# Performance work log

Measured on AMD Instinct MI355X. Metric: run time of the kernel, lower is better.

## Reference

```python
import jax, jax.numpy as jnp
import numpy as np

B, L, D = 4, 4096, 256
INIT_ALPHA = -2.0
INV_TEMP = 1.0 / 0.1


def setup_inputs() -> dict:
    key = jax.random.key(0)
    k1, k2, k3, k4 = jax.random.split(key, 4)
    latents = jax.random.normal(k1, (B, L, D), dtype=jnp.float32)
    current_coords = jax.random.normal(k2, (B, L, 2), dtype=jnp.float32)
    # Linear(D, D, bias=False) weights (torch stores [out, in]; y = x @ W.T)
    lim = 1.0 / np.sqrt(D)
    Wq = jax.random.uniform(k3, (D, D), minval=-lim, maxval=lim, dtype=jnp.float32)
    Wk = jax.random.uniform(k4, (D, D), minval=-lim, maxval=lim, dtype=jnp.float32)
    alpha_raw = jnp.asarray(INIT_ALPHA, dtype=jnp.float32)
    return {"latents": latents, "current_coords": current_coords,
            "Wq": Wq, "Wk": Wk, "alpha_raw": alpha_raw, "layer_idx": 3}


def _l2norm(x, eps=1e-12):
    # F.normalize(dim=-1): x / max(||x||, eps)
    n = jnp.sqrt(jnp.sum(x * x, axis=-1, keepdims=True))
    return x / jnp.maximum(n, eps)


def reference(latents, current_coords, Wq, Wk, alpha_raw, layer_idx):
    # pred_idx selection (share_weights=True): 0 if layer_idx==0 else 1;
    # layer_idx=3 -> params given are for pred_idx=1.
    q = _l2norm(jnp.einsum('bld,ed->ble', latents, Wq))  # [B,L,D]
    k = _l2norm(jnp.einsum('bld,ed->ble', latents, Wk))  # [B,L,D]
    scores = jnp.einsum('bld,bmd->blm', q, k) * INV_TEMP  # [B,L,L]
    scores = jnp.clip(scores, -50.0, 50.0)
    W = jax.nn.softmax(scores, axis=-1)                   # [B,L,L]
    alpha = jax.nn.sigmoid(alpha_raw)
    # M = alpha*W + (1-alpha)*I; M @ coords == alpha*(W@coords) + (1-alpha)*coords
    new_coords = alpha * jnp.einsum('blm,bmc->blc', W, current_coords) \
                 + (1.0 - alpha) * current_coords
    displacement = new_coords - current_coords
    return (new_coords, displacement)
```

## Files before the change

### kernel.cpp

```cpp
#include <hip/hip_runtime.h>
#include <hip/hip_bf16.h>

#define BB 4
#define LL 4096
#define DD 256
#define MM (BB * LL)
#define NSPLIT 4
#define NQB (LL / 128)
#define KPS (LL / NSPLIT)
#define KT 64
#define NKT (KPS / KT)

typedef short short8 __attribute__((ext_vector_type(8)));
typedef float floatx4 __attribute__((ext_vector_type(4)));

#define SCALE_LOG2E 14.426950408889634f

__device__ __forceinline__ unsigned short f2bf(float f) {
    __hip_bfloat16 h = __float2bfloat16(f);
    union { __hip_bfloat16 h; unsigned short s; } c; c.h = h; return c.s;
}

__device__ __forceinline__ float fast_exp2(float x) {
#if __has_builtin(__builtin_amdgcn_exp2f)
    return __builtin_amdgcn_exp2f(x);
#else
    return exp2f(x);
#endif
}

__device__ __forceinline__ void stage16(const char* g, char* l, int lane) {
#if __has_builtin(__builtin_amdgcn_global_load_lds)
    __builtin_amdgcn_global_load_lds(
        (const __attribute__((address_space(1))) void*)(g + lane * 16),
        (__attribute__((address_space(3))) void*)l, 16, 0, 0);
#else
    *(short8*)(l + lane * 16) = *(const short8*)(g + lane * 16);
#endif
}

__global__ __launch_bounds__(256) void cvt_swz_kernel(
    const float* __restrict__ srcq, const float* __restrict__ srck,
    unsigned short* __restrict__ dstq, unsigned short* __restrict__ dstk)
{
    const int which = blockIdx.x >> 5;
    const float* src = which ? srck : srcq;
    unsigned short* dst = which ? dstk : dstq;
    const int t = (blockIdx.x & 31) * 256 + threadIdx.x;
    const int r = t >> 5, c = t & 31;
    const float4 v0 = ((const float4*)src)[t * 2];
    const float4 v1 = ((const float4*)src)[t * 2 + 1];
    short8 o;
    o[0] = (short)f2bf(v0.x); o[1] = (short)f2bf(v0.y);
    o[2] = (short)f2bf(v0.z); o[3] = (short)f2bf(v0.w);
    o[4] = (short)f2bf(v1.x); o[5] = (short)f2bf(v1.y);
    o[6] = (short)f2bf(v1.z); o[7] = (short)f2bf(v1.w);
    const int cs = c ^ (r & 7);
    *(short8*)(dst + (size_t)r * DD + cs * 8) = o;
}

__global__ __launch_bounds__(256) void proj_norm_kernel(
    const float* __restrict__ latents,
    const __hip_bfloat16* __restrict__ Wq,
    const __hip_bfloat16* __restrict__ Wk,
    __hip_bfloat16* __restrict__ qn,
    __hip_bfloat16* __restrict__ kn)
{
    __shared__ char lds[65536];

    const int tid  = threadIdx.x;
    const int wave = tid >> 6;
    const int lane = tid & 63;
    const int n15  = lane & 15;
    const int quad = lane >> 4;
    const int sw   = n15 & 7;

    const int pass  = blockIdx.x & 1;
    const int rbase = (blockIdx.x >> 1) * 64;
    const int m0    = rbase + wave * 16;
    const int r160  = rbase >> 4;

    short8 afrag[8];
    const float* Abase = latents + (size_t)(m0 + n15) * DD + quad * 8;
#pragma unroll
    for (int kk = 0; kk < 8; ++kk) {
        const float4 v0 = *(const float4*)(Abase + kk * 32);
        const float4 v1 = *(const float4*)(Abase + kk * 32 + 4);
        short8 f;
        f[0] = (short)f2bf(v0.x); f[1] = (short)f2bf(v0.y);
        f[2] = (short)f2bf(v0.z); f[3] = (short)f2bf(v0.w);
        f[4] = (short)f2bf(v1.x); f[5] = (short)f2bf(v1.y);
        f[6] = (short)f2bf(v1.z); f[7] = (short)f2bf(v1.w);
        afrag[kk] = f;
    }

    const char* W = (const char*)(pass ? Wk : Wq);

    floatx4 acc[16];
#pragma unroll
    for (int ct = 0; ct < 16; ++ct) acc[ct] = (floatx4){0.f, 0.f, 0.f, 0.f};

    {
        const char* src = W + wave * 8192;
        char* dst = lds + wave * 8192;
#pragma unroll
        for (int j = 0; j < 8; ++j) stage16(src + j * 1024, dst + j * 1024, lane);
    }

    for (int round = 0; round < 4; ++round) {
        __syncthreads();
        if (round + 1 < 4) {
            const char* src = W + (size_t)(round + 1) * 32768 + wave * 8192;
            char* dst = lds + ((round + 1) & 1) * 32768 + wave * 8192;
#pragma unroll
            for (int j = 0; j < 8; ++j) stage16(src + j * 1024, dst + j * 1024, lane);
        }
        const char* buf = lds + (round & 1) * 32768;
#pragma unroll
        for (int jt = 0; jt < 4; ++jt) {
            const int ct = round * 4 + jt;
            const char* lbase = buf + (jt * 16 + n15) * 512;
            floatx4 a = acc[ct];
#pragma unroll
            for (int kk = 0; kk < 8; ++kk) {
                const int chunk = (4 * kk + quad) ^ sw;
                short8 bfr = *(const short8*)(lbase + chunk * 16);
                a = __builtin_amdgcn_mfma_f32_16x16x32_bf16(afrag[kk], bfr, a, 0, 0, 0);
            }
            acc[ct] = a;
        }
    }

    float ss[4] = {0.f, 0.f, 0.f, 0.f};
#pragma unroll
    for (int ct = 0; ct < 16; ++ct)
#pragma unroll
        for (int r = 0; r < 4; ++r) ss[r] += acc[ct][r] * acc[ct][r];
#pragma unroll
    for (int r = 0; r < 4; ++r) {
        ss[r] += __shfl_xor(ss[r], 1, 64);
        ss[r] += __shfl_xor(ss[r], 2, 64);
        ss[r] += __shfl_xor(ss[r], 4, 64);
        ss[r] += __shfl_xor(ss[r], 8, 64);
    }
    float sc[4];
#pragma unroll
    for (int r = 0; r < 4; ++r) {
        sc[r] = 1.f / fmaxf(sqrtf(ss[r]), 1e-12f);
        if (pass == 0) sc[r] *= SCALE_LOG2E;
    }

    unsigned short* tb = (unsigned short*)lds;
#pragma unroll
    for (int h = 0; h < 2; ++h) {
        __syncthreads();
#pragma unroll
        for (int cth = 0; cth < 8; ++cth) {
            const int ct = h * 8 + cth;
            const int col = cth * 16 + n15;
#pragma unroll
            for (int r = 0; r < 4; ++r) {
                const int rl = wave * 16 + quad * 4 + r;
                tb[rl * 136 + col] = f2bf(acc[ct][r] * sc[r]);
            }
        }
        __syncthreads();
        if (pass == 0) {
#pragma unroll
            for (int j = 0; j < 4; ++j) {
                const int g = tid + j * 256;
                const int n15r = g & 15, q2 = (g >> 4) & 3, kkh = (g >> 6) & 3, r16l = (g >> 8) & 3;
                const int rl = r16l * 16 + n15r;
                short8 v = *(const short8*)(tb + rl * 136 + kkh * 32 + q2 * 8);
                const size_t chunk = (((size_t)(r160 + r16l) * 8 + (h * 4 + kkh)) * 4 + q2) * 16 + n15r;
                *(short8*)((char*)qn + chunk * 16) = v;
            }
        } else {
#pragma unroll
            for (int j = 0; j < 4; ++j) {
                const int g = tid + j * 256;
                const int csl = g & 15, rl = g >> 4;
                const int row = rbase + rl;
                const int ci = csl ^ (row & 7);
                short8 v = *(const short8*)(tb + rl * 136 + ci * 8);
                *(short8*)((char*)kn + (size_t)row * 512 + (h * 16 + csl) * 16) = v;
            }
        }
    }
}

__global__ __launch_bounds__(256) void attn_kernel(
    const __hip_bfloat16* __restrict__ qn,
    const __hip_bfloat16* __restrict__ kn,
    const float* __restrict__ coords,
    float* __restrict__ partials)
{
    __shared__ char lds[2 * 32768];

    const int tid  = threadIdx.x;
    const int wave = tid >> 6;
    const int lane = tid & 63;
    const int n15  = lane & 15;
    const int quad = lane >> 4;
    const int sw   = n15 & 7;

    int bs = blockIdx.x;
    const int qb    = bs % NQB;    bs /= NQB;
    const int split = bs % NSPLIT; bs /= NSPLIT;
    const int b     = bs;

    const int mw = b * LL + qb * 128 + wave * 32;

    const int key_base = b * LL + split * KPS;
    const char* ksrc = (const char*)kn + (size_t)key_base * 512;

    {
        const char* src = ksrc + wave * 8192;
        char* dst = lds + wave * 8192;
#pragma unroll
        for (int j = 0; j < 8; ++j) stage16(src + j * 1024, dst + j * 1024, lane);
    }

    short8 aq[2][8];
    const int t16 = mw >> 4;
#pragma unroll
    for (int rt = 0; rt < 2; ++rt)
#pragma unroll
        for (int kk = 0; kk < 8; ++kk) {
            const size_t chunk = (((size_t)(t16 + rt) * 8 + kk) * 4 + quad) * 16 + n15;
            aq[rt][kk] = *(const short8*)((const char*)qn + chunk * 16);
        }

    float s0[2][4], s1[2][4], s2[2][4];
#pragma unroll
    for (int rt = 0; rt < 2; ++rt)
#pragma unroll
        for (int r = 0; r < 4; ++r) { s0[rt][r] = 0.f; s1[rt][r] = 0.f; s2[rt][r] = 0.f; }

    for (int kt = 0; kt < NKT; ++kt) {
        __syncthreads();
        if (kt + 1 < NKT) {
            const char* src = ksrc + (size_t)(kt + 1) * KT * 512 + wave * 8192;
            char* dst = lds + ((kt + 1) & 1) * 32768 + wave * 8192;
#pragma unroll
            for (int j = 0; j < 8; ++j) stage16(src + j * 1024, dst + j * 1024, lane);
        }
        const char* buf = lds + (kt & 1) * 32768;

#pragma unroll
        for (int ct = 0; ct < 4; ++ct) {
            const int kidx = key_base + kt * KT + ct * 16 + n15;
            const float2 cc = *(const float2*)(coords + (size_t)kidx * 2);

            floatx4 acc0 = (floatx4){0.f, 0.f, 0.f, 0.f};
            floatx4 acc1 = (floatx4){0.f, 0.f, 0.f, 0.f};
            const char* lbase = buf + (ct * 16 + n15) * 512;
#pragma unroll
            for (int kk = 0; kk < 8; ++kk) {
                const int chunk = (4 * kk + quad) ^ sw;
                short8 bfr = *(const short8*)(lbase + chunk * 16);
                acc0 = __builtin_amdgcn_mfma_f32_16x16x32_bf16(aq[0][kk], bfr, acc0, 0, 0, 0);
                acc1 = __builtin_amdgcn_mfma_f32_16x16x32_bf16(aq[1][kk], bfr, acc1, 0, 0, 0);
            }
#pragma unroll
            for (int r = 0; r < 4; ++r) {
                const float e0 = fast_exp2(acc0[r]);
                const float e1 = fast_exp2(acc1[r]);
                s0[0][r] += e0;
                s1[0][r] = fmaf(cc.x, e0, s1[0][r]);
                s2[0][r] = fmaf(cc.y, e0, s2[0][r]);
                s0[1][r] += e1;
                s1[1][r] = fmaf(cc.x, e1, s1[1][r]);
                s2[1][r] = fmaf(cc.y, e1, s2[1][r]);
            }
        }
    }

#pragma unroll
    for (int rt = 0; rt < 2; ++rt)
#pragma unroll
        for (int r = 0; r < 4; ++r)
#pragma unroll
            for (int mask = 1; mask <= 8; mask <<= 1) {
                s0[rt][r] += __shfl_xor(s0[rt][r], mask, 64);
                s1[rt][r] += __shfl_xor(s1[rt][r], mask, 64);
                s2[rt][r] += __shfl_xor(s2[rt][r], mask, 64);
            }

    if (n15 == 0) {
#pragma unroll
        for (int rt = 0; rt < 2; ++rt)
#pragma unroll
            for (int r = 0; r < 4; ++r) {
                const int m = mw + rt * 16 + quad * 4 + r;
                float* p = partials + ((size_t)split * MM + m) * 4;
                p[0] = s0[rt][r];
                p[1] = s1[rt][r];
                p[2] = s2[rt][r];
            }
    }
}

__global__ __launch_bounds__(256) void finish_kernel(
    const float* __restrict__ partials,
    const float* __restrict__ coords,
    const float* __restrict__ alpha_raw,
    float* __restrict__ out)
{
    const int m = blockIdx.x * 256 + threadIdx.x;

    const float alpha = 1.f / (1.f + __expf(-alpha_raw[0]));

    float s0 = 0.f, s1 = 0.f, s2 = 0.f;
#pragma unroll
    for (int s = 0; s < NSPLIT; ++s) {
        const float4 v = *(const float4*)(partials + ((size_t)s * MM + m) * 4);
        s0 += v.x; s1 += v.y; s2 += v.z;
    }

    const float cx = coords[m * 2];
    const float cy = coords[m * 2 + 1];
    const float inv = 1.f / s0;
    const float nx = alpha * (s1 * inv) + (1.f - alpha) * cx;
    const float ny = alpha * (s2 * inv) + (1.f - alpha) * cy;

    out[m * 2]     = nx;
    out[m * 2 + 1] = ny;
    out[2 * MM + m * 2]     = nx - cx;
    out[2 * MM + m * 2 + 1] = ny - cy;
}

extern "C" void kernel_launch(void* const* d_in, const int* in_sizes, int n_in,
                              void* d_out, int out_size, void* d_ws, size_t ws_size,
                              hipStream_t stream) {
    const float* latents   = (const float*)d_in[0];
    const float* coords    = (const float*)d_in[1];
    const float* Wq        = (const float*)d_in[2];
    const float* Wk        = (const float*)d_in[3];
    const float* alpha_raw = (const float*)d_in[4];

    char* ws = (char*)d_ws;
    __hip_bfloat16* qn   = (__hip_bfloat16*)ws;
    __hip_bfloat16* kn   = (__hip_bfloat16*)(ws + (size_t)8 * 1024 * 1024);
    __hip_bfloat16* wq_b = (__hip_bfloat16*)(ws + (size_t)16 * 1024 * 1024);
    __hip_bfloat16* wk_b = (__hip_bfloat16*)(ws + (size_t)16 * 1024 * 1024 + 131072);
    float* partials      = (float*)(ws + (size_t)16 * 1024 * 1024 + 262144);

    float* out = (float*)d_out;

    cvt_swz_kernel<<<64, 256, 0, stream>>>(Wq, Wk, (unsigned short*)wq_b, (unsigned short*)wk_b);
    proj_norm_kernel<<<512, 256, 0, stream>>>(latents, wq_b, wk_b, qn, kn);
    attn_kernel<<<BB * NQB * NSPLIT, 256, 0, stream>>>(qn, kn, coords, partials);
    finish_kernel<<<MM / 256, 256, 0, stream>>>(partials, coords, alpha_raw, out);
}
```

Baseline: 124.9 us.

## Read projection weights directly from global and double attention key splits

The projection kernel stops staging swizzled weights through a 64KB LDS double buffer. Each wave now reads bf16 weight rows straight from global memory (L2-resident), and the weight conversion kernel drops the swizzle. The attention kernel doubles the key splits to 8 and halves the key tile to 32, which doubles the grid and halves LDS per block to raise occupancy. The risk is more partials for the finish kernel to reduce and uncoalesced global loads of B fragments in the projection.

```diff
diff --git a/kernel.cpp b/kernel.cpp
--- a/kernel.cpp
+++ b/kernel.cpp
@@ -5,10 +5,10 @@
 #define LL 4096
 #define DD 256
 #define MM (BB * LL)
-#define NSPLIT 4
+#define NSPLIT 8
 #define NQB (LL / 128)
 #define KPS (LL / NSPLIT)
-#define KT 64
+#define KT 32
 #define NKT (KPS / KT)
 
 typedef short short8 __attribute__((ext_vector_type(8)));
@@ -39,7 +39,7 @@
 #endif
 }
 
-__global__ __launch_bounds__(256) void cvt_swz_kernel(
+__global__ __launch_bounds__(256) void cvt_kernel(
     const float* __restrict__ srcq, const float* __restrict__ srck,
     unsigned short* __restrict__ dstq, unsigned short* __restrict__ dstk)
 {
@@ -47,7 +47,6 @@
     const float* src = which ? srck : srcq;
     unsigned short* dst = which ? dstk : dstq;
     const int t = (blockIdx.x & 31) * 256 + threadIdx.x;
-    const int r = t >> 5, c = t & 31;
     const float4 v0 = ((const float4*)src)[t * 2];
     const float4 v1 = ((const float4*)src)[t * 2 + 1];
     short8 o;
@@ -55,8 +54,7 @@
     o[2] = (short)f2bf(v0.z); o[3] = (short)f2bf(v0.w);
     o[4] = (short)f2bf(v1.x); o[5] = (short)f2bf(v1.y);
     o[6] = (short)f2bf(v1.z); o[7] = (short)f2bf(v1.w);
-    const int cs = c ^ (r & 7);
-    *(short8*)(dst + (size_t)r * DD + cs * 8) = o;
+    *(short8*)(dst + (size_t)t * 8) = o;
 }
 
 __global__ __launch_bounds__(256) void proj_norm_kernel(
@@ -66,14 +64,13 @@
     __hip_bfloat16* __restrict__ qn,
     __hip_bfloat16* __restrict__ kn)
 {
-    __shared__ char lds[65536];
+    __shared__ unsigned short tb[64 * 136];
 
     const int tid  = threadIdx.x;
     const int wave = tid >> 6;
     const int lane = tid & 63;
     const int n15  = lane & 15;
     const int quad = lane >> 4;
-    const int sw   = n15 & 7;
 
     const int pass  = blockIdx.x & 1;
     const int rbase = (blockIdx.x >> 1) * 64;
@@ -94,41 +91,22 @@
         afrag[kk] = f;
     }
 
-    const char* W = (const char*)(pass ? Wk : Wq);
+    const short* W = (const short*)(pass ? Wk : Wq);
 
     floatx4 acc[16];
 #pragma unroll
     for (int ct = 0; ct < 16; ++ct) acc[ct] = (floatx4){0.f, 0.f, 0.f, 0.f};
 
-    {
-        const char* src = W + wave * 8192;
-        char* dst = lds + wave * 8192;
-#pragma unroll
-        for (int j = 0; j < 8; ++j) stage16(src + j * 1024, dst + j * 1024, lane);
-    }
-
-    for (int round = 0; round < 4; ++round) {
-        __syncthreads();
-        if (round + 1 < 4) {
-            const char* src = W + (size_t)(round + 1) * 32768 + wave * 8192;
-            char* dst = lds + ((round + 1) & 1) * 32768 + wave * 8192;
-#pragma unroll
-            for (int j = 0; j < 8; ++j) stage16(src + j * 1024, dst + j * 1024, lane);
-        }
-        const char* buf = lds + (round & 1) * 32768;
-#pragma unroll
-        for (int jt = 0; jt < 4; ++jt) {
-            const int ct = round * 4 + jt;
-            const char* lbase = buf + (jt * 16 + n15) * 512;
-            floatx4 a = acc[ct];
-#pragma unroll
-            for (int kk = 0; kk < 8; ++kk) {
-                const int chunk = (4 * kk + quad) ^ sw;
-                short8 bfr = *(const short8*)(lbase + chunk * 16);
-                a = __builtin_amdgcn_mfma_f32_16x16x32_bf16(afrag[kk], bfr, a, 0, 0, 0);
-            }
-            acc[ct] = a;
-        }
+#pragma unroll
+    for (int ct = 0; ct < 16; ++ct) {
+        const short* Brow = W + (size_t)(ct * 16 + n15) * DD + quad * 8;
+        floatx4 a = acc[ct];
+#pragma unroll
+        for (int kk = 0; kk < 8; ++kk) {
+            short8 bfr = *(const short8*)(Brow + kk * 32);
+            a = __builtin_amdgcn_mfma_f32_16x16x32_bf16(afrag[kk], bfr, a, 0, 0, 0);
+        }
+        acc[ct] = a;
     }
 
     float ss[4] = {0.f, 0.f, 0.f, 0.f};
@@ -150,7 +128,6 @@
         if (pass == 0) sc[r] *= SCALE_LOG2E;
     }
 
-    unsigned short* tb = (unsigned short*)lds;
 #pragma unroll
     for (int h = 0; h < 2; ++h) {
         __syncthreads();
@@ -195,7 +172,7 @@
     const float* __restrict__ coords,
     float* __restrict__ partials)
 {
-    __shared__ char lds[2 * 32768];
+    __shared__ char lds[2 * 16384];
 
     const int tid  = threadIdx.x;
     const int wave = tid >> 6;
@@ -215,10 +192,10 @@
     const char* ksrc = (const char*)kn + (size_t)key_base * 512;
 
     {
-        const char* src = ksrc + wave * 8192;
-        char* dst = lds + wave * 8192;
-#pragma unroll
-        for (int j = 0; j < 8; ++j) stage16(src + j * 1024, dst + j * 1024, lane);
+        const char* src = ksrc + wave * 4096;
+        char* dst = lds + wave * 4096;
+#pragma unroll
+        for (int j = 0; j < 4; ++j) stage16(src + j * 1024, dst + j * 1024, lane);
     }
 
     short8 aq[2][8];
@@ -240,15 +217,15 @@
     for (int kt = 0; kt < NKT; ++kt) {
         __syncthreads();
         if (kt + 1 < NKT) {
-            const char* src = ksrc + (size_t)(kt + 1) * KT * 512 + wave * 8192;
-            char* dst = lds + ((kt + 1) & 1) * 32768 + wave * 8192;
-#pragma unroll
-            for (int j = 0; j < 8; ++j) stage16(src + j * 1024, dst + j * 1024, lane);
-        }
-        const char* buf = lds + (kt & 1) * 32768;
-
-#pragma unroll
-        for (int ct = 0; ct < 4; ++ct) {
+            const char* src = ksrc + (size_t)(kt + 1) * KT * 512 + wave * 4096;
+            char* dst = lds + ((kt + 1) & 1) * 16384 + wave * 4096;
+#pragma unroll
+            for (int j = 0; j < 4; ++j) stage16(src + j * 1024, dst + j * 1024, lane);
+        }
+        const char* buf = lds + (kt & 1) * 16384;
+
+#pragma unroll
+        for (int ct = 0; ct < 2; ++ct) {
             const int kidx = key_base + kt * KT + ct * 16 + n15;
             const float2 cc = *(const float2*)(coords + (size_t)kidx * 2);
 
@@ -348,7 +325,7 @@
 
     float* out = (float*)d_out;
 
-    cvt_swz_kernel<<<64, 256, 0, stream>>>(Wq, Wk, (unsigned short*)wq_b, (unsigned short*)wk_b);
+    cvt_kernel<<<64, 256, 0, stream>>>(Wq, Wk, (unsigned short*)wq_b, (unsigned short*)wk_b);
     proj_norm_kernel<<<512, 256, 0, stream>>>(latents, wq_b, wk_b, qn, kn);
     attn_kernel<<<BB * NQB * NSPLIT, 256, 0, stream>>>(qn, kn, coords, partials);
     finish_kernel<<<MM / 256, 256, 0, stream>>>(partials, coords, alpha_raw, out);
```

Result: slower. 152.9 us (+22.4%).

## Process 64 query rows per wave to reuse LDS key fragments across four MFMA tiles

Applied to the files above, without the earlier changes.

Each wave now computes 4 query row-tiles (64 rows) instead of 2 against every key fragment read from LDS. This halves LDS traffic per MFMA and amortizes the coordinate loads. The key-split count is doubled so the grid size stays the same. Launch bounds request 2 blocks per SM, since the larger Q-fragment and accumulator arrays raise register pressure and could cause spills or lower occupancy.

```diff
diff --git a/kernel.cpp b/kernel.cpp
--- a/kernel.cpp
+++ b/kernel.cpp
@@ -5,8 +5,9 @@
 #define LL 4096
 #define DD 256
 #define MM (BB * LL)
-#define NSPLIT 4
-#define NQB (LL / 128)
+#define NSPLIT 8
+#define BM 256
+#define NQB (LL / BM)
 #define KPS (LL / NSPLIT)
 #define KT 64
 #define NKT (KPS / KT)
@@ -189,7 +190,7 @@
     }
 }
 
-__global__ __launch_bounds__(256) void attn_kernel(
+__global__ __launch_bounds__(256, 2) void attn_kernel(
     const __hip_bfloat16* __restrict__ qn,
     const __hip_bfloat16* __restrict__ kn,
     const float* __restrict__ coords,
@@ -209,7 +210,7 @@
     const int split = bs % NSPLIT; bs /= NSPLIT;
     const int b     = bs;
 
-    const int mw = b * LL + qb * 128 + wave * 32;
+    const int mw = b * LL + qb * BM + wave * 64;
 
     const int key_base = b * LL + split * KPS;
     const char* ksrc = (const char*)kn + (size_t)key_base * 512;
@@ -221,19 +222,19 @@
         for (int j = 0; j < 8; ++j) stage16(src + j * 1024, dst + j * 1024, lane);
     }
 
-    short8 aq[2][8];
+    short8 aq[4][8];
     const int t16 = mw >> 4;
 #pragma unroll
-    for (int rt = 0; rt < 2; ++rt)
+    for (int rt = 0; rt < 4; ++rt)
 #pragma unroll
         for (int kk = 0; kk < 8; ++kk) {
             const size_t chunk = (((size_t)(t16 + rt) * 8 + kk) * 4 + quad) * 16 + n15;
             aq[rt][kk] = *(const short8*)((const char*)qn + chunk * 16);
         }
 
-    float s0[2][4], s1[2][4], s2[2][4];
-#pragma unroll
-    for (int rt = 0; rt < 2; ++rt)
+    float s0[4][4], s1[4][4], s2[4][4];
+#pragma unroll
+    for (int rt = 0; rt < 4; ++rt)
 #pragma unroll
         for (int r = 0; r < 4; ++r) { s0[rt][r] = 0.f; s1[rt][r] = 0.f; s2[rt][r] = 0.f; }
 
@@ -252,32 +253,32 @@
             const int kidx = key_base + kt * KT + ct * 16 + n15;
             const float2 cc = *(const float2*)(coords + (size_t)kidx * 2);
 
-            floatx4 acc0 = (floatx4){0.f, 0.f, 0.f, 0.f};
-            floatx4 acc1 = (floatx4){0.f, 0.f, 0.f, 0.f};
+            floatx4 acc[4];
+#pragma unroll
+            for (int rt = 0; rt < 4; ++rt) acc[rt] = (floatx4){0.f, 0.f, 0.f, 0.f};
             const char* lbase = buf + (ct * 16 + n15) * 512;
 #pragma unroll
             for (int kk = 0; kk < 8; ++kk) {
                 const int chunk = (4 * kk + quad) ^ sw;
                 short8 bfr = *(const short8*)(lbase + chunk * 16);
-                acc0 = __builtin_amdgcn_mfma_f32_16x16x32_bf16(aq[0][kk], bfr, acc0, 0, 0, 0);
-                acc1 = __builtin_amdgcn_mfma_f32_16x16x32_bf16(aq[1][kk], bfr, acc1, 0, 0, 0);
-            }
-#pragma unroll
-            for (int r = 0; r < 4; ++r) {
-                const float e0 = fast_exp2(acc0[r]);
-                const float e1 = fast_exp2(acc1[r]);
-                s0[0][r] += e0;
-                s1[0][r] = fmaf(cc.x, e0, s1[0][r]);
-                s2[0][r] = fmaf(cc.y, e0, s2[0][r]);
-                s0[1][r] += e1;
-                s1[1][r] = fmaf(cc.x, e1, s1[1][r]);
-                s2[1][r] = fmaf(cc.y, e1, s2[1][r]);
-            }
-        }
-    }
-
-#pragma unroll
-    for (int rt = 0; rt < 2; ++rt)
+#pragma unroll
+                for (int rt = 0; rt < 4; ++rt)
+                    acc[rt] = __builtin_amdgcn_mfma_f32_16x16x32_bf16(aq[rt][kk], bfr, acc[rt], 0, 0, 0);
+            }
+#pragma unroll
+            for (int rt = 0; rt < 4; ++rt)
+#pragma unroll
+                for (int r = 0; r < 4; ++r) {
+                    const float e = fast_exp2(acc[rt][r]);
+                    s0[rt][r] += e;
+                    s1[rt][r] = fmaf(cc.x, e, s1[rt][r]);
+                    s2[rt][r] = fmaf(cc.y, e, s2[rt][r]);
+                }
+        }
+    }
+
+#pragma unroll
+    for (int rt = 0; rt < 4; ++rt)
 #pragma unroll
         for (int r = 0; r < 4; ++r)
 #pragma unroll
@@ -289,7 +290,7 @@
 
     if (n15 == 0) {
 #pragma unroll
-        for (int rt = 0; rt < 2; ++rt)
+        for (int rt = 0; rt < 4; ++rt)
 #pragma unroll
             for (int r = 0; r < 4; ++r) {
                 const int m = mw + rt * 16 + quad * 4 + r;
```

Measured after the change: 123.2 us. About the same (-1.4%).
